# Optimization experiments

Measured on AMD Instinct MI355X. Metric: run time of the kernel, lower is better.

The kernel has to match this reference:

```python
import jax, jax.numpy as jnp
import numpy as np

NUM_HEADS_SPLIT = 12   # hardcoded in einops reduce pattern
NUM_HEADS_SCALE = 8    # num_heads used only for scale computation (module bug, kept faithful)


def setup_inputs() -> dict:
    key = jax.random.key(0)
    ks = jax.random.split(key, 5)
    B, P, D = 32, 577, 768
    return {
        "x": jax.random.normal(ks[0], (B, P, D), dtype=jnp.float32),
        "qkv_w": jax.random.normal(ks[1], (3 * D, D), dtype=jnp.float32) * 0.02,
        "qkv_b": jax.random.normal(ks[2], (3 * D,), dtype=jnp.float32) * 0.02,
        "out_w": jax.random.normal(ks[3], (D, D), dtype=jnp.float32) * 0.02,
        "out_b": jax.random.normal(ks[4], (D,), dtype=jnp.float32) * 0.02,
    }


def reference(x, qkv_w, qkv_b, out_w, out_b):
    B, P, D = x.shape
    h = NUM_HEADS_SPLIT
    s = D // h
    scale = (D // NUM_HEADS_SCALE) ** -0.5  # 96**-0.5, per original code

    # qkv projection: [B, P, 3D]
    qkv = jnp.einsum('bpd,ed->bpe', x, qkv_w) + qkv_b
    # reshape 'b p (c h s) -> b p c h s' (reduce with mean is a pure reshape here)
    qkv = qkv.reshape(B, P, 3, h, s)
    # split order in the original: v, q, k
    v = jnp.transpose(qkv[:, :, 0], (0, 2, 1, 3))  # [B, h, P, s]
    q = jnp.transpose(qkv[:, :, 1], (0, 2, 1, 3))
    k = jnp.transpose(qkv[:, :, 2], (0, 2, 1, 3))

    attn = jnp.einsum('bhps,bhqs->bhpq', q, k) * scale
    attn = jax.nn.softmax(attn, axis=-1)
    out = jnp.einsum('bhpq,bhqs->bhps', attn, v)  # [B, h, P, s]
    out = jnp.transpose(out, (0, 2, 1, 3)).reshape(B, P, D)

    return jnp.einsum('bpd,ed->bpe', out, out_w) + out_b
```

## Files before the change

### kernel.cpp

```cpp
#include <hip/hip_runtime.h>
#include <stdint.h>

typedef __attribute__((ext_vector_type(8))) short short8;
typedef __attribute__((ext_vector_type(4))) float floatx4;

#define DEV static __device__ __forceinline__

constexpr int Bb = 32, Pp = 577, Dd = 768, Hh = 12;
constexpr int M_VALID = Bb * Pp;
constexpr int M_PAD   = 18560;
constexpr int PKV     = 640;
constexpr float SCALE = 0.10206207261596577f;

DEV ushort f2b(float f) {
  union { float f; uint32_t u; } c; c.f = f;
  uint32_t u = c.u + 0x7fffu + ((c.u >> 16) & 1u);
  return (ushort)(u >> 16);
}

__global__ void cvt_pad(const float* __restrict__ src, ushort* __restrict__ dst,
                        int n_valid4, int n_total4) {
  const float4* s4 = (const float4*)src;
  for (int i = blockIdx.x * blockDim.x + threadIdx.x; i < n_total4;
       i += gridDim.x * blockDim.x) {
    float4 v = make_float4(0.f, 0.f, 0.f, 0.f);
    if (i < n_valid4) v = s4[i];
    ushort4 o;
    o.x = f2b(v.x); o.y = f2b(v.y); o.z = f2b(v.z); o.w = f2b(v.w);
    ((ushort4*)dst)[i] = o;
  }
}

#define STAGE(bi, kk)                                                          \
  do {                                                                         \
    __builtin_amdgcn_global_load_lds(                                          \
        (const __attribute__((address_space(1))) void*)(gA0 + (kk)),           \
        (__attribute__((address_space(3))) void*)(As + (bi)*4096 + tid * 8),   \
        16, 0, 0);                                                             \
    __builtin_amdgcn_global_load_lds(                                          \
        (const __attribute__((address_space(1))) void*)(gA1 + (kk)),           \
        (__attribute__((address_space(3))) void*)(As + (bi)*4096 + 2048 + tid * 8), \
        16, 0, 0);                                                             \
    __builtin_amdgcn_global_load_lds(                                          \
        (const __attribute__((address_space(1))) void*)(gB0 + (kk)),           \
        (__attribute__((address_space(3))) void*)(Bs + (bi)*4096 + tid * 8),   \
        16, 0, 0);                                                             \
    __builtin_amdgcn_global_load_lds(                                          \
        (const __attribute__((address_space(1))) void*)(gB1 + (kk)),           \
        (__attribute__((address_space(3))) void*)(Bs + (bi)*4096 + 2048 + tid * 8), \
        16, 0, 0);                                                             \
  } while (0)

template<bool C_F32>
__global__ __launch_bounds__(256) void gemm_bt(
    const ushort* __restrict__ A, int lda,
    const ushort* __restrict__ Bw,
    const float* __restrict__ bias, void* __restrict__ Cout,
    int N, int K, int m_valid, int nt_n)
{
  __shared__ ushort As[2 * 128 * 32];
  __shared__ ushort Bs[2 * 128 * 32];
  const int tid = threadIdx.x;
  const int lane = tid & 63;
  const int w = tid >> 6;
  const int wr = w >> 1, wc = w & 1;
  const int llo = lane & 15, lhi = lane >> 4;

  {
  }
  const int nwg = gridDim.x;
  const int L = blockIdx.x;
  const int q = nwg >> 3, r = nwg & 7;
  const int xcd = L & 7, pos = L >> 3;
  const int wgid = (xcd < r ? xcd * (q + 1) : r * (q + 1) + (xcd - r) * q) + pos;
  const int m0 = (wgid / nt_n) * 128, n0 = (wgid % nt_n) * 128;

  floatx4 acc[4][4];
#pragma unroll
  for (int i = 0; i < 4; ++i)
#pragma unroll
    for (int j = 0; j < 4; ++j) acc[i][j] = floatx4{0.f, 0.f, 0.f, 0.f};

  const int srow = tid >> 2;
  const int scol = (tid & 3) * 8;
  const ushort* gA0 = A  + (size_t)(m0 + srow) * lda + scol;
  const ushort* gA1 = A  + (size_t)(m0 + 64 + srow) * lda + scol;
  const ushort* gB0 = Bw + (size_t)(n0 + srow) * K + scol;
  const ushort* gB1 = Bw + (size_t)(n0 + 64 + srow) * K + scol;

  STAGE(0, 0);
  int cur = 0;
  for (int kk = 0; kk < K; kk += 32) {
    if (kk + 32 < K) {
      STAGE(cur ^ 1, kk + 32);
      asm volatile("s_waitcnt vmcnt(4)" ::: "memory");
    } else {
      asm volatile("s_waitcnt vmcnt(0)" ::: "memory");
    }
    __builtin_amdgcn_s_barrier();
    __builtin_amdgcn_sched_barrier(0);

    const ushort* Ab = As + cur * 4096;
    const ushort* Bb = Bs + cur * 4096;
    short8 af[4], bfr[4];
#pragma unroll
    for (int i = 0; i < 4; ++i) {
      af[i]  = *(const short8*)(Ab + (wr * 64 + i * 16 + llo) * 32 + lhi * 8);
      bfr[i] = *(const short8*)(Bb + (wc * 64 + i * 16 + llo) * 32 + lhi * 8);
    }
#pragma unroll
    for (int i = 0; i < 4; ++i)
#pragma unroll
      for (int j = 0; j < 4; ++j)
        acc[i][j] = __builtin_amdgcn_mfma_f32_16x16x32_bf16(af[i], bfr[j], acc[i][j], 0, 0, 0);

    __builtin_amdgcn_sched_barrier(0);
    __builtin_amdgcn_s_barrier();
    cur ^= 1;
  }

  float bv[4];
#pragma unroll
  for (int j = 0; j < 4; ++j) bv[j] = bias[n0 + wc * 64 + j * 16 + llo];

#pragma unroll
  for (int i = 0; i < 4; ++i) {
#pragma unroll
    for (int r2 = 0; r2 < 4; ++r2) {
      const int row = m0 + wr * 64 + i * 16 + lhi * 4 + r2;
      if (C_F32 && row >= m_valid) continue;
      const size_t rb = (size_t)row * N + n0 + wc * 64;
#pragma unroll
      for (int j = 0; j < 4; ++j) {
        float v = acc[i][j][r2] + bv[j];
        if (C_F32) ((float*)Cout)[rb + j * 16 + llo] = v;
        else       ((ushort*)Cout)[rb + j * 16 + llo] = f2b(v);
      }
    }
  }
}

__global__ __launch_bounds__(256) void vtrans(const ushort* __restrict__ C1,
                                              ushort* __restrict__ Vt) {
  const int pt = blockIdx.x, h = blockIdx.y, b = blockIdx.z;
  __shared__ ushort Ts[64][72];
  const int t = threadIdx.x;
  const int rl = t >> 2, c16 = (t & 3) * 16;
  const int p = pt * 64 + rl;
  short8 a0 = {0,0,0,0,0,0,0,0}, a1 = {0,0,0,0,0,0,0,0};
  if (p < Pp) {
    const ushort* s = C1 + (size_t)(b * Pp + p) * 2304 + h * 64 + c16;
    a0 = *(const short8*)s;
    a1 = *(const short8*)(s + 8);
  }
  *(short8*)&Ts[rl][c16] = a0;
  *(short8*)&Ts[rl][c16 + 8] = a1;
  __syncthreads();
  const int ss = t >> 2, pc16 = (t & 3) * 16;
  short8 o0, o1;
#pragma unroll
  for (int i = 0; i < 8; ++i) {
    o0[i] = (short)Ts[pc16 + i][ss];
    o1[i] = (short)Ts[pc16 + 8 + i][ss];
  }
  ushort* d = Vt + ((size_t)(b * Hh + h) * 64 + ss) * PKV + pt * 64 + pc16;
  *(short8*)d = o0;
  *(short8*)(d + 8) = o1;
}

__global__ __launch_bounds__(256) void attn_fwd(
    ushort* C1, const ushort* __restrict__ Vt)
{
  const int qt = blockIdx.x, h = blockIdx.y, b = blockIdx.z;
  const int tid = threadIdx.x;
  const int lane = tid & 63, w = tid >> 6;
  const int llo = lane & 15, lhi = lane >> 4;

  __shared__ ushort Ks[64][72];
  __shared__ ushort Vs[64][72];
  __shared__ ushort Ps[4][16][72];

  const int q0 = qt * 64;
  const int qrow = q0 + w * 16 + llo;
  const size_t qoff = (size_t)(b * Pp + qrow) * 2304 + 768 + h * 64;
  const short8 qf0 = *(const short8*)(C1 + qoff + lhi * 8);
  const short8 qf1 = *(const short8*)(C1 + qoff + 32 + lhi * 8);

  float ls[4] = {0.f, 0.f, 0.f, 0.f};
  floatx4 acc_o[4];
#pragma unroll
  for (int st = 0; st < 4; ++st) acc_o[st] = floatx4{0.f, 0.f, 0.f, 0.f};

  const int srow = tid >> 2;
  const int sc16 = (tid & 3) * 16;
  const ushort* kbase = C1 + (size_t)(b * Pp + srow) * 2304 + 1536 + h * 64 + sc16;
  const ushort* vbase = Vt + ((size_t)(b * Hh + h) * 64 + srow) * PKV + sc16;

  for (int t = 0; t < 10; ++t) {
    const short8 k0 = *(const short8*)(kbase + (size_t)t * 64 * 2304);
    const short8 k1 = *(const short8*)(kbase + (size_t)t * 64 * 2304 + 8);
    const short8 v0 = *(const short8*)(vbase + t * 64);
    const short8 v1 = *(const short8*)(vbase + t * 64 + 8);
    __syncthreads();
    *(short8*)&Ks[srow][sc16] = k0;
    *(short8*)&Ks[srow][sc16 + 8] = k1;
    *(short8*)&Vs[srow][sc16] = v0;
    *(short8*)&Vs[srow][sc16 + 8] = v1;
    __syncthreads();

    float pv[4][4];
#pragma unroll
    for (int ntl = 0; ntl < 4; ++ntl) {
      floatx4 acc = floatx4{0.f, 0.f, 0.f, 0.f};
      const short8 bf0 = *(const short8*)&Ks[ntl * 16 + llo][lhi * 8];
      const short8 bf1 = *(const short8*)&Ks[ntl * 16 + llo][32 + lhi * 8];
      acc = __builtin_amdgcn_mfma_f32_16x16x32_bf16(qf0, bf0, acc, 0, 0, 0);
      acc = __builtin_amdgcn_mfma_f32_16x16x32_bf16(qf1, bf1, acc, 0, 0, 0);
      const bool valid = (t * 64 + ntl * 16 + llo) < Pp;
#pragma unroll
      for (int r = 0; r < 4; ++r) {
        const float p = valid ? __expf(acc[r] * SCALE) : 0.f;
        pv[ntl][r] = p;
        ls[r] += p;
      }
    }

#pragma unroll
    for (int r = 0; r < 4; ++r)
#pragma unroll
      for (int ntl = 0; ntl < 4; ++ntl)
        Ps[w][lhi * 4 + r][ntl * 16 + llo] = f2b(pv[ntl][r]);

    const short8 pa0 = *(const short8*)&Ps[w][llo][lhi * 8];
    const short8 pa1 = *(const short8*)&Ps[w][llo][32 + lhi * 8];
#pragma unroll
    for (int st = 0; st < 4; ++st) {
      const short8 vb0 = *(const short8*)&Vs[st * 16 + llo][lhi * 8];
      const short8 vb1 = *(const short8*)&Vs[st * 16 + llo][32 + lhi * 8];
      acc_o[st] = __builtin_amdgcn_mfma_f32_16x16x32_bf16(pa0, vb0, acc_o[st], 0, 0, 0);
      acc_o[st] = __builtin_amdgcn_mfma_f32_16x16x32_bf16(pa1, vb1, acc_o[st], 0, 0, 0);
    }
  }

#pragma unroll
  for (int r = 0; r < 4; ++r) {
#pragma unroll
    for (int off = 1; off < 16; off <<= 1) ls[r] += __shfl_xor(ls[r], off, 64);
  }

#pragma unroll
  for (int r = 0; r < 4; ++r) {
    const int p = q0 + w * 16 + lhi * 4 + r;
    if (p < Pp) {
      const float inv = 1.f / ls[r];
      const size_t ob = (size_t)(b * Pp + p) * 2304 + h * 64;
#pragma unroll
      for (int st = 0; st < 4; ++st)
        C1[ob + st * 16 + llo] = f2b(acc_o[st][r] * inv);
    }
  }
}

extern "C" void kernel_launch(void* const* d_in, const int* in_sizes, int n_in,
                              void* d_out, int out_size, void* d_ws, size_t ws_size,
                              hipStream_t stream) {
  const float* x     = (const float*)d_in[0];
  const float* qkv_w = (const float*)d_in[1];
  const float* qkv_b = (const float*)d_in[2];
  const float* out_w = (const float*)d_in[3];
  const float* out_b = (const float*)d_in[4];
  float* out = (float*)d_out;

  char* ws = (char*)d_ws;
  ushort* C1b = (ushort*)(ws);
  ushort* W3b = (ushort*)(ws + 85524480);
  ushort* W1b = (ushort*)(ws + 86704128);
  ushort* Xb  = (ushort*)(ws + 90243072);
  ushort* Vtb = (ushort*)(ws + 86704128);

  cvt_pad<<<2048, 256, 0, stream>>>(x, Xb, M_VALID * 768 / 4, M_PAD * 768 / 4);
  cvt_pad<<<1024, 256, 0, stream>>>(qkv_w, W1b, 2304 * 768 / 4, 2304 * 768 / 4);
  cvt_pad<<<512, 256, 0, stream>>>(out_w, W3b, 768 * 768 / 4, 768 * 768 / 4);

  gemm_bt<false><<<dim3(145 * 18), 256, 0, stream>>>(Xb, 768, W1b, qkv_b,
                                                     (void*)C1b, 2304, 768, M_PAD, 18);
  vtrans<<<dim3(10, 12, 32), 256, 0, stream>>>(C1b, Vtb);
  attn_fwd<<<dim3(10, 12, 32), 256, 0, stream>>>(C1b, Vtb);
  gemm_bt<true><<<dim3(145 * 6), 256, 0, stream>>>(C1b, 2304, W3b, out_b,
                                                   (void*)out, 768, 768, M_VALID, 6);
}
```

Measured before the change: 350.9 us.

## Triple-buffer GEMM loads and widen attention blocks with register prefetch

```diff
diff --git a/kernel.cpp b/kernel.cpp
--- a/kernel.cpp
+++ b/kernel.cpp
@@ -11,6 +11,7 @@
 constexpr int M_PAD   = 18560;
 constexpr int PKV     = 640;
 constexpr float SCALE = 0.10206207261596577f;
+constexpr float SCALE_LOG2E = 0.10206207261596577f * 1.4426950408889634f;
 
 DEV ushort f2b(float f) {
   union { float f; uint32_t u; } c; c.f = f;
@@ -58,16 +59,14 @@
     const float* __restrict__ bias, void* __restrict__ Cout,
     int N, int K, int m_valid, int nt_n)
 {
-  __shared__ ushort As[2 * 128 * 32];
-  __shared__ ushort Bs[2 * 128 * 32];
+  __shared__ ushort As[3 * 128 * 32];
+  __shared__ ushort Bs[3 * 128 * 32];
   const int tid = threadIdx.x;
   const int lane = tid & 63;
   const int w = tid >> 6;
   const int wr = w >> 1, wc = w & 1;
   const int llo = lane & 15, lhi = lane >> 4;
 
-  {
-  }
   const int nwg = gridDim.x;
   const int L = blockIdx.x;
   const int q = nwg >> 3, r = nwg & 7;
@@ -89,10 +88,14 @@
   const ushort* gB1 = Bw + (size_t)(n0 + 64 + srow) * K + scol;
 
   STAGE(0, 0);
+  STAGE(1, 32);
   int cur = 0;
   for (int kk = 0; kk < K; kk += 32) {
-    if (kk + 32 < K) {
-      STAGE(cur ^ 1, kk + 32);
+    if (kk + 64 < K) {
+      int b2 = cur + 2; if (b2 >= 3) b2 -= 3;
+      STAGE(b2, kk + 64);
+      asm volatile("s_waitcnt vmcnt(8)" ::: "memory");
+    } else if (kk + 32 < K) {
       asm volatile("s_waitcnt vmcnt(4)" ::: "memory");
     } else {
       asm volatile("s_waitcnt vmcnt(0)" ::: "memory");
@@ -101,12 +104,12 @@
     __builtin_amdgcn_sched_barrier(0);
 
     const ushort* Ab = As + cur * 4096;
-    const ushort* Bb = Bs + cur * 4096;
+    const ushort* Bbp = Bs + cur * 4096;
     short8 af[4], bfr[4];
 #pragma unroll
     for (int i = 0; i < 4; ++i) {
       af[i]  = *(const short8*)(Ab + (wr * 64 + i * 16 + llo) * 32 + lhi * 8);
-      bfr[i] = *(const short8*)(Bb + (wc * 64 + i * 16 + llo) * 32 + lhi * 8);
+      bfr[i] = *(const short8*)(Bbp + (wc * 64 + i * 16 + llo) * 32 + lhi * 8);
     }
 #pragma unroll
     for (int i = 0; i < 4; ++i)
@@ -116,7 +119,7 @@
 
     __builtin_amdgcn_sched_barrier(0);
     __builtin_amdgcn_s_barrier();
-    cur ^= 1;
+    cur += 1; if (cur >= 3) cur -= 3;
   }
 
   float bv[4];
@@ -168,7 +171,7 @@
   *(short8*)(d + 8) = o1;
 }
 
-__global__ __launch_bounds__(256) void attn_fwd(
+__global__ __launch_bounds__(512) void attn_fwd(
     ushort* C1, const ushort* __restrict__ Vt)
 {
   const int qt = blockIdx.x, h = blockIdx.y, b = blockIdx.z;
@@ -178,9 +181,9 @@
 
   __shared__ ushort Ks[64][72];
   __shared__ ushort Vs[64][72];
-  __shared__ ushort Ps[4][16][72];
-
-  const int q0 = qt * 64;
+  __shared__ ushort Ps[8][16][72];
+
+  const int q0 = qt * 128;
   const int qrow = q0 + w * 16 + llo;
   const size_t qoff = (size_t)(b * Pp + qrow) * 2304 + 768 + h * 64;
   const short8 qf0 = *(const short8*)(C1 + qoff + lhi * 8);
@@ -191,21 +194,22 @@
 #pragma unroll
   for (int st = 0; st < 4; ++st) acc_o[st] = floatx4{0.f, 0.f, 0.f, 0.f};
 
-  const int srow = tid >> 2;
-  const int sc16 = (tid & 3) * 16;
-  const ushort* kbase = C1 + (size_t)(b * Pp + srow) * 2304 + 1536 + h * 64 + sc16;
-  const ushort* vbase = Vt + ((size_t)(b * Hh + h) * 64 + srow) * PKV + sc16;
+  const int srow = tid >> 3;
+  const int sc8 = (tid & 7) * 8;
+  const ushort* kbase = C1 + (size_t)(b * Pp + srow) * 2304 + 1536 + h * 64 + sc8;
+  const ushort* vbase = Vt + ((size_t)(b * Hh + h) * 64 + srow) * PKV + sc8;
+
+  short8 kc = *(const short8*)(kbase);
+  short8 vc = *(const short8*)(vbase);
 
   for (int t = 0; t < 10; ++t) {
-    const short8 k0 = *(const short8*)(kbase + (size_t)t * 64 * 2304);
-    const short8 k1 = *(const short8*)(kbase + (size_t)t * 64 * 2304 + 8);
-    const short8 v0 = *(const short8*)(vbase + t * 64);
-    const short8 v1 = *(const short8*)(vbase + t * 64 + 8);
     __syncthreads();
-    *(short8*)&Ks[srow][sc16] = k0;
-    *(short8*)&Ks[srow][sc16 + 8] = k1;
-    *(short8*)&Vs[srow][sc16] = v0;
-    *(short8*)&Vs[srow][sc16 + 8] = v1;
+    *(short8*)&Ks[srow][sc8] = kc;
+    *(short8*)&Vs[srow][sc8] = vc;
+    if (t < 9) {
+      kc = *(const short8*)(kbase + (size_t)(t + 1) * 64 * 2304);
+      vc = *(const short8*)(vbase + (t + 1) * 64);
+    }
     __syncthreads();
 
     float pv[4][4];
@@ -219,7 +223,7 @@
       const bool valid = (t * 64 + ntl * 16 + llo) < Pp;
 #pragma unroll
       for (int r = 0; r < 4; ++r) {
-        const float p = valid ? __expf(acc[r] * SCALE) : 0.f;
+        const float p = valid ? exp2f(acc[r] * SCALE_LOG2E) : 0.f;
         pv[ntl][r] = p;
         ls[r] += p;
       }
@@ -285,7 +289,7 @@
   gemm_bt<false><<<dim3(145 * 18), 256, 0, stream>>>(Xb, 768, W1b, qkv_b,
                                                      (void*)C1b, 2304, 768, M_PAD, 18);
   vtrans<<<dim3(10, 12, 32), 256, 0, stream>>>(C1b, Vtb);
-  attn_fwd<<<dim3(10, 12, 32), 256, 0, stream>>>(C1b, Vtb);
+  attn_fwd<<<dim3(5, 12, 32), 512, 0, stream>>>(C1b, Vtb);
   gemm_bt<true><<<dim3(145 * 6), 256, 0, stream>>>(C1b, 2304, W3b, out_b,
                                                    (void*)out, 768, 768, M_VALID, 6);
 }
```

New measurement: 355.4 us. No clear change (+1.3%).
